# Kernel optimization log

Hardware: AMD Instinct MI355X
Metric: run time of the kernel (lower is better)

Reference implementation:

```python
import jax, jax.numpy as jnp
import numpy as np

NEG = 10000.0

def setup_inputs() -> dict:
    key = jax.random.key(0)
    ks = jax.random.split(key, 5)
    B, S, D = 2, 2048, 1024
    std = 1.0 / np.sqrt(D)
    return {
        "x": jax.random.normal(ks[0], (B, S, D), dtype=jnp.float32),
        "Wq": jax.random.normal(ks[1], (D, D), dtype=jnp.float32) * std,
        "bq": jnp.zeros((D,), jnp.float32),
        "Wk": jax.random.normal(ks[2], (D, D), dtype=jnp.float32) * std,
        "bk": jnp.zeros((D,), jnp.float32),
        "Wv": jax.random.normal(ks[3], (D, D), dtype=jnp.float32) * std,
        "bv": jnp.zeros((D,), jnp.float32),
        "Wo": jax.random.normal(ks[4], (D, D), dtype=jnp.float32) * std,
        "bo": jnp.zeros((D,), jnp.float32),
    }

def reference(x, Wq, bq, Wk, bk, Wv, bv, Wo, bo):
    # Linear projections + relu activation (as in the keras layer; note: no head split
    # is performed in this implementation, head_num is only a divisibility check).
    q = jax.nn.relu(x @ Wq + bq)  # [B,S,D]
    k = jax.nn.relu(x @ Wk + bk)
    v = jax.nn.relu(x @ Wv + bv)
    D = q.shape[-1]
    e = jnp.einsum('bqd,bkd->bqk', q, k) / jnp.sqrt(jnp.float32(D))  # [B,S,S]
    # history_only causal mask: penalize key positions j > query position i
    S = e.shape[-1]
    causal = (jnp.arange(S)[None, :] > jnp.arange(S)[:, None]).astype(e.dtype)
    e = e - NEG * causal[None, :, :]
    # stable softmax exactly as in the source (max-subtract, exp, normalize)
    e = jnp.exp(e - jnp.max(e, axis=-1, keepdims=True))
    attn = e / jnp.sum(e, axis=-1, keepdims=True)
    y = jnp.einsum('bqk,bkd->bqd', attn, v)
    return jax.nn.relu(y @ Wo + bo)
```

## Files before the change

kernel.cpp:

```cpp
#include <hip/hip_runtime.h>
#include <math.h>


typedef _Float16 f16x8 __attribute__((ext_vector_type(8)));
typedef float f32x4 __attribute__((ext_vector_type(4)));

#define BK 64

__device__ __forceinline__ void gload_lds16(const void* g, void* l) {
  __builtin_amdgcn_global_load_lds(
      (const __attribute__((address_space(1))) void*)g,
      (__attribute__((address_space(3))) void*)l, 16, 0, 0);
}

template<bool RELU, bool HAS_BIAS, int CAUSAL, int TMp, int TNp, bool MULTI, typename OT>
__global__ __launch_bounds__(256) void gemm_f16(
    const _Float16* __restrict__ A, const _Float16* __restrict__ BT,
    const float* __restrict__ bias0, const float* __restrict__ bias1,
    const float* __restrict__ bias2,
    OT* __restrict__ C0, OT* __restrict__ C1, OT* __restrict__ C2,
    int M, int Nout, int K, float scale,
    long long sA, long long sB, long long sC)
{
  int m0, n0;
  if (CAUSAL == 1) {
    int bx = blockIdx.x;
    int i = (int)((sqrtf(4.f * bx + 1.f) - 1.f) * 0.5f);
    while ((i + 1) * (i + 2) <= bx) ++i;
    while (i * (i + 1) > bx) --i;
    int j = bx - i * (i + 1);
    m0 = i * TMp;
    n0 = j * TNp;
  } else {
    m0 = blockIdx.y * TMp;
    n0 = blockIdx.x * TNp;
  }
  A  += (long long)blockIdx.z * sA;
  BT += (long long)blockIdx.z * sB;
  const int kend = (CAUSAL == 2) ? ((m0 + TMp < K) ? m0 + TMp : K) : K;

  __shared__ _Float16 Ah[TMp * BK];
  __shared__ _Float16 Bh[TNp * BK];

  const int tid  = threadIdx.x;
  const int lane = tid & 63;
  const int wid  = tid >> 6;
  const int wm   = (wid >> 1) * (TMp / 2);
  const int wn   = (wid & 1) * (TNp / 2);
  const int l15  = lane & 15;
  const int quad = lane >> 4;
  constexpr int MT = TMp / 32;
  constexpr int NT = TNp / 32;

  f32x4 acc[MT][NT];
  #pragma unroll
  for (int i = 0; i < MT; ++i)
    #pragma unroll
    for (int j = 0; j < NT; ++j)
      acc[i][j] = (f32x4){0.f, 0.f, 0.f, 0.f};

  constexpr int AI = TMp / 32;
  constexpr int BI = TNp / 32;
  const int rl8  = lane >> 3;
  const int swk  = ((lane & 7) ^ rl8) * 8;
  const int arow = wid * (TMp / 4);
  const int brow = wid * (TNp / 4);

  for (int k0 = 0; k0 < kend; k0 += BK) {
    #pragma unroll
    for (int t = 0; t < AI; ++t)
      gload_lds16(A + (long long)(m0 + arow + t * 8 + rl8) * K + k0 + swk,
                  Ah + (arow + t * 8) * BK);
    #pragma unroll
    for (int t = 0; t < BI; ++t)
      gload_lds16(BT + (long long)(n0 + brow + t * 8 + rl8) * K + k0 + swk,
                  Bh + (brow + t * 8) * BK);
    __syncthreads();

    const _Float16* ab = Ah + (wm + l15) * BK;
    const _Float16* bb = Bh + (wn + l15) * BK;
    const int sw8 = l15 & 7;
    #pragma unroll
    for (int ko = 0; ko < 2; ++ko) {
      const int ch = ((ko * 4 + quad) ^ sw8) * 8;
      f16x8 af[MT], bf[NT];
      #pragma unroll
      for (int t = 0; t < MT; ++t) af[t] = *(const f16x8*)(ab + t * 16 * BK + ch);
      #pragma unroll
      for (int t = 0; t < NT; ++t) bf[t] = *(const f16x8*)(bb + t * 16 * BK + ch);
      #pragma unroll
      for (int mt = 0; mt < MT; ++mt)
        #pragma unroll
        for (int nt = 0; nt < NT; ++nt)
          acc[mt][nt] = __builtin_amdgcn_mfma_f32_16x16x32_f16(
              af[mt], bf[nt], acc[mt][nt], 0, 0, 0);
    }
    __syncthreads();
  }

  const int mat = MULTI ? (n0 / Nout) : 0;
  const float* bias = HAS_BIAS ? (mat == 0 ? bias0 : (mat == 1 ? bias1 : bias2)) : nullptr;
  OT* C = (mat == 0 ? C0 : (mat == 1 ? C1 : C2)) + (long long)blockIdx.z * sC;
  const int c0 = MULTI ? (n0 - mat * Nout) : n0;

  float bvals[NT];
  if (HAS_BIAS) {
    #pragma unroll
    for (int nt = 0; nt < NT; ++nt)
      bvals[nt] = bias[c0 + wn + nt * 16 + l15];
  }
  #pragma unroll
  for (int mt = 0; mt < MT; ++mt) {
    #pragma unroll
    for (int nt = 0; nt < NT; ++nt) {
      const int col = c0 + wn + nt * 16 + l15;
      #pragma unroll
      for (int r = 0; r < 4; ++r) {
        const int row = m0 + wm + mt * 16 + quad * 4 + r;
        float v = acc[mt][nt][r] * scale;
        if (HAS_BIAS) v += bvals[nt];
        if (RELU) v = fmaxf(v, 0.f);
        C[(long long)row * Nout + col] = (OT)v;
      }
    }
  }
}

__global__ __launch_bounds__(256) void cvt_f32_f16(
    const float* __restrict__ in, _Float16* __restrict__ out)
{
  const long long i = ((long long)blockIdx.x * 256 + threadIdx.x) * 8;
  float4 a = *(const float4*)(in + i);
  float4 b = *(const float4*)(in + i + 4);
  f16x8 o = {(_Float16)a.x, (_Float16)a.y, (_Float16)a.z, (_Float16)a.w,
             (_Float16)b.x, (_Float16)b.y, (_Float16)b.z, (_Float16)b.w};
  *(f16x8*)(out + i) = o;
}

__global__ __launch_bounds__(256) void cvtT_all(
    const float* __restrict__ W0, const float* __restrict__ W1,
    const float* __restrict__ W2, const float* __restrict__ W3,
    _Float16* __restrict__ WT, int K, int N)
{
  __shared__ _Float16 t[64][72];
  const int z = blockIdx.z;
  const float* W = (z == 0) ? W0 : (z == 1) ? W1 : (z == 2) ? W2 : W3;
  _Float16* dst = WT + (long long)z * K * N;
  const int k0 = blockIdx.x * 64, n0 = blockIdx.y * 64;
  const int tid = threadIdx.x;
  #pragma unroll
  for (int it = 0; it < 4; ++it) {
    int idx = tid + it * 256;
    int r = idx >> 4, c4 = (idx & 15) << 2;
    float4 w = *(const float4*)(W + (long long)(k0 + r) * N + n0 + c4);
    t[r][c4 + 0] = (_Float16)w.x; t[r][c4 + 1] = (_Float16)w.y;
    t[r][c4 + 2] = (_Float16)w.z; t[r][c4 + 3] = (_Float16)w.w;
  }
  __syncthreads();
  #pragma unroll
  for (int it = 0; it < 2; ++it) {
    int idx = tid + it * 256;
    int r = idx >> 3, c8 = (idx & 7) << 3;
    f16x8 o;
    #pragma unroll
    for (int j = 0; j < 8; ++j) o[j] = t[c8 + j][r];
    *(f16x8*)(dst + (long long)(n0 + r) * K + k0 + c8) = o;
  }
}

__global__ __launch_bounds__(256) void softmax_causal_h(
    _Float16* __restrict__ E, int S)
{
  const int i = blockIdx.x;
  _Float16* row = E + ((long long)blockIdx.y * S + i) * S;
  const int tid = threadIdx.x;
  const int n = i + 1;
  const int j0 = tid * 8;

  f16x8 hv = *(const f16x8*)(row + j0);
  float vals[8];
  float m = -3.0e38f;
  #pragma unroll
  for (int t = 0; t < 8; ++t) {
    float v = (j0 + t < n) ? (float)hv[t] : -3.0e38f;
    vals[t] = v;
    m = fmaxf(m, v);
  }
  #pragma unroll
  for (int o = 32; o > 0; o >>= 1) m = fmaxf(m, __shfl_down(m, o, 64));

  __shared__ float rmax[4];
  __shared__ float rsum[4];
  const int wave = tid >> 6;
  if ((tid & 63) == 0) rmax[wave] = m;
  __syncthreads();
  m = fmaxf(fmaxf(rmax[0], rmax[1]), fmaxf(rmax[2], rmax[3]));

  float s = 0.f;
  #pragma unroll
  for (int t = 0; t < 8; ++t) {
    float e = (j0 + t < n) ? expf(vals[t] - m) : 0.f;
    vals[t] = e;
    s += e;
  }
  #pragma unroll
  for (int o = 32; o > 0; o >>= 1) s += __shfl_down(s, o, 64);
  if ((tid & 63) == 0) rsum[wave] = s;
  __syncthreads();
  s = rsum[0] + rsum[1] + rsum[2] + rsum[3];

  const float inv = 1.0f / s;
  f16x8 ov;
  #pragma unroll
  for (int t = 0; t < 8; ++t) ov[t] = (_Float16)(vals[t] * inv);
  *(f16x8*)(row + j0) = ov;
}

extern "C" void kernel_launch(void* const* d_in, const int* in_sizes, int n_in,
                              void* d_out, int out_size, void* d_ws, size_t ws_size,
                              hipStream_t stream) {
  const float* x  = (const float*)d_in[0];
  const float* Wq = (const float*)d_in[1];
  const float* bq = (const float*)d_in[2];
  const float* Wk = (const float*)d_in[3];
  const float* bk = (const float*)d_in[4];
  const float* Wv = (const float*)d_in[5];
  const float* bv = (const float*)d_in[6];
  const float* Wo = (const float*)d_in[7];
  const float* bo = (const float*)d_in[8];
  float* out = (float*)d_out;

  const int Bn = 2, S = 2048, D = 1024;
  const int M = Bn * S;
  const size_t MD = (size_t)M * D;
  const size_t DD = (size_t)D * D;
  const size_t SS = (size_t)Bn * S * S;

  _Float16* ws   = (_Float16*)d_ws;
  _Float16* xh   = ws;
  _Float16* Wcat = xh + MD;
  _Float16* Qh   = Wcat + 4 * DD;
  _Float16* Kh   = Qh + MD;
  _Float16* Vh   = Kh + MD;
  _Float16* VWT  = Vh + MD;
  _Float16* E    = VWT + MD;

  dim3 blk(256);

  cvt_f32_f16<<<dim3((unsigned)(MD / 2048)), blk, 0, stream>>>(x, xh);
  cvtT_all<<<dim3(D / 64, D / 64, 4), blk, 0, stream>>>(Wq, Wk, Wv, Wo, Wcat, D, D);

  gemm_f16<true, true, 0, 128, 128, true, _Float16>
      <<<dim3(3 * D / 128, M / 128), blk, 0, stream>>>(
      xh, Wcat, bq, bk, bv, Qh, Kh, Vh, M, D, D, 1.0f, 0, 0, 0);

  gemm_f16<false, false, 1, 128, 64, false, _Float16>
      <<<dim3(272, 1, Bn), blk, 0, stream>>>(
      Qh, Kh, nullptr, nullptr, nullptr, E, nullptr, nullptr,
      S, S, D, 0.03125f, (long long)S * D, (long long)S * D, (long long)S * S);

  gemm_f16<false, false, 0, 128, 64, false, _Float16>
      <<<dim3(S / 64, D / 128, Bn), blk, 0, stream>>>(
      Wcat + 3 * DD, Vh, nullptr, nullptr, nullptr, VWT, nullptr, nullptr,
      D, S, D, 1.0f, 0, (long long)S * D, (long long)D * S);

  softmax_causal_h<<<dim3(S, Bn), blk, 0, stream>>>(E, S);

  gemm_f16<true, true, 2, 64, 128, false, float>
      <<<dim3(D / 128, S / 64, Bn), blk, 0, stream>>>(
      E, VWT, bo, nullptr, nullptr, out, nullptr, nullptr,
      S, D, S, 1.0f, (long long)S * S, (long long)D * S, (long long)S * D);
}
```

Baseline: 209.3 us.

## Merge launches into fused multi-role kernels and halve GEMM K-tile to 32

```diff
diff --git a/kernel.cpp b/kernel.cpp
--- a/kernel.cpp
+++ b/kernel.cpp
@@ -5,7 +5,7 @@
 typedef _Float16 f16x8 __attribute__((ext_vector_type(8)));
 typedef float f32x4 __attribute__((ext_vector_type(4)));
 
-#define BK 64
+#define BK 32
 
 __device__ __forceinline__ void gload_lds16(const void* g, void* l) {
   __builtin_amdgcn_global_load_lds(
@@ -13,35 +13,12 @@
       (__attribute__((address_space(3))) void*)l, 16, 0, 0);
 }
 
-template<bool RELU, bool HAS_BIAS, int CAUSAL, int TMp, int TNp, bool MULTI, typename OT>
-__global__ __launch_bounds__(256) void gemm_f16(
+template<int TMp, int TNp>
+__device__ __forceinline__ void gemm_acc(
     const _Float16* __restrict__ A, const _Float16* __restrict__ BT,
-    const float* __restrict__ bias0, const float* __restrict__ bias1,
-    const float* __restrict__ bias2,
-    OT* __restrict__ C0, OT* __restrict__ C1, OT* __restrict__ C2,
-    int M, int Nout, int K, float scale,
-    long long sA, long long sB, long long sC)
-{
-  int m0, n0;
-  if (CAUSAL == 1) {
-    int bx = blockIdx.x;
-    int i = (int)((sqrtf(4.f * bx + 1.f) - 1.f) * 0.5f);
-    while ((i + 1) * (i + 2) <= bx) ++i;
-    while (i * (i + 1) > bx) --i;
-    int j = bx - i * (i + 1);
-    m0 = i * TMp;
-    n0 = j * TNp;
-  } else {
-    m0 = blockIdx.y * TMp;
-    n0 = blockIdx.x * TNp;
-  }
-  A  += (long long)blockIdx.z * sA;
-  BT += (long long)blockIdx.z * sB;
-  const int kend = (CAUSAL == 2) ? ((m0 + TMp < K) ? m0 + TMp : K) : K;
-
-  __shared__ _Float16 Ah[TMp * BK];
-  __shared__ _Float16 Bh[TNp * BK];
-
+    _Float16* Ah, _Float16* Bh, int sAr, int sBr, int kend, int m0, int n0,
+    f32x4 (&acc)[TMp / 32][TNp / 32])
+{
   const int tid  = threadIdx.x;
   const int lane = tid & 63;
   const int wid  = tid >> 6;
@@ -51,69 +28,68 @@
   const int quad = lane >> 4;
   constexpr int MT = TMp / 32;
   constexpr int NT = TNp / 32;
-
-  f32x4 acc[MT][NT];
-  #pragma unroll
-  for (int i = 0; i < MT; ++i)
-    #pragma unroll
-    for (int j = 0; j < NT; ++j)
-      acc[i][j] = (f32x4){0.f, 0.f, 0.f, 0.f};
-
-  constexpr int AI = TMp / 32;
-  constexpr int BI = TNp / 32;
-  const int rl8  = lane >> 3;
-  const int swk  = ((lane & 7) ^ rl8) * 8;
+  constexpr int AI = TMp / 64;
+  constexpr int BI = TNp / 64;
+  const int r16 = lane >> 2;
+  const int swc = ((lane & 3) ^ ((lane >> 3) & 3)) * 8;
   const int arow = wid * (TMp / 4);
   const int brow = wid * (TNp / 4);
 
   for (int k0 = 0; k0 < kend; k0 += BK) {
     #pragma unroll
     for (int t = 0; t < AI; ++t)
-      gload_lds16(A + (long long)(m0 + arow + t * 8 + rl8) * K + k0 + swk,
-                  Ah + (arow + t * 8) * BK);
+      gload_lds16(A + (long long)(m0 + arow + t * 16 + r16) * sAr + k0 + swc,
+                  Ah + (arow + t * 16) * BK);
     #pragma unroll
     for (int t = 0; t < BI; ++t)
-      gload_lds16(BT + (long long)(n0 + brow + t * 8 + rl8) * K + k0 + swk,
-                  Bh + (brow + t * 8) * BK);
+      gload_lds16(BT + (long long)(n0 + brow + t * 16 + r16) * sBr + k0 + swc,
+                  Bh + (brow + t * 16) * BK);
     __syncthreads();
 
-    const _Float16* ab = Ah + (wm + l15) * BK;
-    const _Float16* bb = Bh + (wn + l15) * BK;
-    const int sw8 = l15 & 7;
-    #pragma unroll
-    for (int ko = 0; ko < 2; ++ko) {
-      const int ch = ((ko * 4 + quad) ^ sw8) * 8;
-      f16x8 af[MT], bf[NT];
+    const int ch = (quad ^ ((l15 >> 1) & 3)) * 8;
+    const _Float16* ab = Ah + (wm + l15) * BK + ch;
+    const _Float16* bb = Bh + (wn + l15) * BK + ch;
+    f16x8 af[MT], bf[NT];
+    #pragma unroll
+    for (int t = 0; t < MT; ++t) af[t] = *(const f16x8*)(ab + t * 16 * BK);
+    #pragma unroll
+    for (int t = 0; t < NT; ++t) bf[t] = *(const f16x8*)(bb + t * 16 * BK);
+    #pragma unroll
+    for (int mt = 0; mt < MT; ++mt)
       #pragma unroll
-      for (int t = 0; t < MT; ++t) af[t] = *(const f16x8*)(ab + t * 16 * BK + ch);
-      #pragma unroll
-      for (int t = 0; t < NT; ++t) bf[t] = *(const f16x8*)(bb + t * 16 * BK + ch);
-      #pragma unroll
-      for (int mt = 0; mt < MT; ++mt)
-        #pragma unroll
-        for (int nt = 0; nt < NT; ++nt)
-          acc[mt][nt] = __builtin_amdgcn_mfma_f32_16x16x32_f16(
-              af[mt], bf[nt], acc[mt][nt], 0, 0, 0);
-    }
+      for (int nt = 0; nt < NT; ++nt)
+        acc[mt][nt] = __builtin_amdgcn_mfma_f32_16x16x32_f16(
+            af[mt], bf[nt], acc[mt][nt], 0, 0, 0);
     __syncthreads();
   }
-
-  const int mat = MULTI ? (n0 / Nout) : 0;
-  const float* bias = HAS_BIAS ? (mat == 0 ? bias0 : (mat == 1 ? bias1 : bias2)) : nullptr;
-  OT* C = (mat == 0 ? C0 : (mat == 1 ? C1 : C2)) + (long long)blockIdx.z * sC;
-  const int c0 = MULTI ? (n0 - mat * Nout) : n0;
+}
+
+template<int TMp, int TNp, bool RELU, bool HAS_BIAS, typename OT>
+__device__ __forceinline__ void gemm_store(
+    f32x4 (&acc)[TMp / 32][TNp / 32], const float* __restrict__ bias,
+    OT* __restrict__ C, int Nout, float scale, int m0, int n0)
+{
+  const int tid  = threadIdx.x;
+  const int lane = tid & 63;
+  const int wid  = tid >> 6;
+  const int wm   = (wid >> 1) * (TMp / 2);
+  const int wn   = (wid & 1) * (TNp / 2);
+  const int l15  = lane & 15;
+  const int quad = lane >> 4;
+  constexpr int MT = TMp / 32;
+  constexpr int NT = TNp / 32;
 
   float bvals[NT];
   if (HAS_BIAS) {
     #pragma unroll
     for (int nt = 0; nt < NT; ++nt)
-      bvals[nt] = bias[c0 + wn + nt * 16 + l15];
+      bvals[nt] = bias[n0 + wn + nt * 16 + l15];
   }
   #pragma unroll
   for (int mt = 0; mt < MT; ++mt) {
     #pragma unroll
     for (int nt = 0; nt < NT; ++nt) {
-      const int col = c0 + wn + nt * 16 + l15;
+      const int col = n0 + wn + nt * 16 + l15;
       #pragma unroll
       for (int r = 0; r < 4; ++r) {
         const int row = m0 + wm + mt * 16 + quad * 4 + r;
@@ -126,33 +102,132 @@
   }
 }
 
-__global__ __launch_bounds__(256) void cvt_f32_f16(
-    const float* __restrict__ in, _Float16* __restrict__ out)
-{
-  const long long i = ((long long)blockIdx.x * 256 + threadIdx.x) * 8;
-  float4 a = *(const float4*)(in + i);
-  float4 b = *(const float4*)(in + i + 4);
-  f16x8 o = {(_Float16)a.x, (_Float16)a.y, (_Float16)a.z, (_Float16)a.w,
-             (_Float16)b.x, (_Float16)b.y, (_Float16)b.z, (_Float16)b.w};
-  *(f16x8*)(out + i) = o;
-}
-
-__global__ __launch_bounds__(256) void cvtT_all(
+__global__ __launch_bounds__(256) void qkv_kernel(
+    const _Float16* __restrict__ xh, const _Float16* __restrict__ Wcat,
+    const float* __restrict__ bq, const float* __restrict__ bk,
+    const float* __restrict__ bv,
+    _Float16* __restrict__ Qh, _Float16* __restrict__ Kh,
+    _Float16* __restrict__ Vh, int D)
+{
+  __shared__ _Float16 Ah[128 * BK];
+  __shared__ _Float16 Bh[128 * BK];
+  const int m0  = blockIdx.y * 128;
+  const int n0g = blockIdx.x * 128;
+  f32x4 acc[4][4];
+  #pragma unroll
+  for (int i = 0; i < 4; ++i)
+    #pragma unroll
+    for (int j = 0; j < 4; ++j) acc[i][j] = (f32x4){0.f, 0.f, 0.f, 0.f};
+
+  gemm_acc<128, 128>(xh, Wcat, Ah, Bh, D, D, D, m0, n0g, acc);
+
+  const int mat = n0g >> 10;
+  const int c0  = n0g & 1023;
+  _Float16* C = (mat == 0) ? Qh : (mat == 1) ? Kh : Vh;
+  const float* bias = (mat == 0) ? bq : (mat == 1) ? bk : bv;
+  gemm_store<128, 128, true, true, _Float16>(acc, bias, C, D, 1.0f, m0, c0);
+}
+
+__global__ __launch_bounds__(256) void mid_kernel(
+    const _Float16* __restrict__ Qh, const _Float16* __restrict__ Kh,
+    _Float16* __restrict__ E, const _Float16* __restrict__ WoT,
+    const _Float16* __restrict__ Vh, _Float16* __restrict__ VWT,
+    int S, int D)
+{
+  __shared__ _Float16 Ah[128 * BK];
+  __shared__ _Float16 Bh[64 * BK];
+  const _Float16 *A, *BT;
+  _Float16* C;
+  int m0, n0;
+  float scale;
+  const int id = blockIdx.x;
+  if (id < 544) {
+    const int z = (id >= 272);
+    const int t = id - z * 272;
+    int i = (int)((sqrtf(4.f * t + 1.f) - 1.f) * 0.5f);
+    while ((i + 1) * (i + 2) <= t) ++i;
+    while (i * (i + 1) > t) --i;
+    const int j = t - i * (i + 1);
+    m0 = i * 128;
+    n0 = j * 64;
+    A  = Qh + (long long)z * S * D;
+    BT = Kh + (long long)z * S * D;
+    C  = E + (long long)z * S * S;
+    scale = 0.03125f;
+  } else {
+    const int t = id - 544;
+    const int z = t >> 8;
+    const int u = t & 255;
+    m0 = (u >> 5) * 128;
+    n0 = (u & 31) * 64;
+    A  = WoT;
+    BT = Vh + (long long)z * S * D;
+    C  = VWT + (long long)z * D * S;
+    scale = 1.0f;
+  }
+  f32x4 acc[4][2];
+  #pragma unroll
+  for (int i = 0; i < 4; ++i)
+    #pragma unroll
+    for (int j = 0; j < 2; ++j) acc[i][j] = (f32x4){0.f, 0.f, 0.f, 0.f};
+
+  gemm_acc<128, 64>(A, BT, Ah, Bh, D, D, D, m0, n0, acc);
+  gemm_store<128, 64, false, false, _Float16>(acc, nullptr, C, S, scale, m0, n0);
+}
+
+__global__ __launch_bounds__(256) void pv_kernel(
+    const _Float16* __restrict__ E, const _Float16* __restrict__ VWT,
+    const float* __restrict__ bo, float* __restrict__ out, int S, int D)
+{
+  __shared__ _Float16 Ah[64 * BK];
+  __shared__ _Float16 Bh[128 * BK];
+  const int z  = blockIdx.z;
+  const int m0 = ((int)gridDim.y - 1 - (int)blockIdx.y) * 64;
+  const int n0 = blockIdx.x * 128;
+  const _Float16* A  = E + (long long)z * S * S;
+  const _Float16* BT = VWT + (long long)z * D * S;
+  float* C = out + (long long)z * S * D;
+  const int kend = m0 + 64;
+
+  f32x4 acc[2][4];
+  #pragma unroll
+  for (int i = 0; i < 2; ++i)
+    #pragma unroll
+    for (int j = 0; j < 4; ++j) acc[i][j] = (f32x4){0.f, 0.f, 0.f, 0.f};
+
+  gemm_acc<64, 128>(A, BT, Ah, Bh, S, S, kend, m0, n0, acc);
+  gemm_store<64, 128, true, true, float>(acc, bo, C, D, 1.0f, m0, n0);
+}
+
+__global__ __launch_bounds__(256) void prep_kernel(
+    const float* __restrict__ x, _Float16* __restrict__ xh,
     const float* __restrict__ W0, const float* __restrict__ W1,
     const float* __restrict__ W2, const float* __restrict__ W3,
-    _Float16* __restrict__ WT, int K, int N)
-{
+    _Float16* __restrict__ Wcat, int D)
+{
+  const int id = blockIdx.x;
+  const int tid = threadIdx.x;
+  if (id < 2048) {
+    const long long i = ((long long)id * 256 + tid) * 8;
+    float4 a = *(const float4*)(x + i);
+    float4 b = *(const float4*)(x + i + 4);
+    f16x8 o = {(_Float16)a.x, (_Float16)a.y, (_Float16)a.z, (_Float16)a.w,
+               (_Float16)b.x, (_Float16)b.y, (_Float16)b.z, (_Float16)b.w};
+    *(f16x8*)(xh + i) = o;
+    return;
+  }
   __shared__ _Float16 t[64][72];
-  const int z = blockIdx.z;
+  const int u = id - 2048;
+  const int z = u >> 8;
+  const int v = u & 255;
   const float* W = (z == 0) ? W0 : (z == 1) ? W1 : (z == 2) ? W2 : W3;
-  _Float16* dst = WT + (long long)z * K * N;
-  const int k0 = blockIdx.x * 64, n0 = blockIdx.y * 64;
-  const int tid = threadIdx.x;
+  _Float16* dst = Wcat + (long long)z * D * D;
+  const int k0 = (v >> 4) * 64, n0 = (v & 15) * 64;
   #pragma unroll
   for (int it = 0; it < 4; ++it) {
     int idx = tid + it * 256;
     int r = idx >> 4, c4 = (idx & 15) << 2;
-    float4 w = *(const float4*)(W + (long long)(k0 + r) * N + n0 + c4);
+    float4 w = *(const float4*)(W + (long long)(k0 + r) * D + n0 + c4);
     t[r][c4 + 0] = (_Float16)w.x; t[r][c4 + 1] = (_Float16)w.y;
     t[r][c4 + 2] = (_Float16)w.z; t[r][c4 + 3] = (_Float16)w.w;
   }
@@ -164,7 +239,7 @@
     f16x8 o;
     #pragma unroll
     for (int j = 0; j < 8; ++j) o[j] = t[c8 + j][r];
-    *(f16x8*)(dst + (long long)(n0 + r) * K + k0 + c8) = o;
+    *(f16x8*)(dst + (long long)(n0 + r) * D + k0 + c8) = o;
   }
 }
 
@@ -247,27 +322,16 @@
 
   dim3 blk(256);
 
-  cvt_f32_f16<<<dim3((unsigned)(MD / 2048)), blk, 0, stream>>>(x, xh);
-  cvtT_all<<<dim3(D / 64, D / 64, 4), blk, 0, stream>>>(Wq, Wk, Wv, Wo, Wcat, D, D);
-
-  gemm_f16<true, true, 0, 128, 128, true, _Float16>
-      <<<dim3(3 * D / 128, M / 128), blk, 0, stream>>>(
-      xh, Wcat, bq, bk, bv, Qh, Kh, Vh, M, D, D, 1.0f, 0, 0, 0);
-
-  gemm_f16<false, false, 1, 128, 64, false, _Float16>
-      <<<dim3(272, 1, Bn), blk, 0, stream>>>(
-      Qh, Kh, nullptr, nullptr, nullptr, E, nullptr, nullptr,
-      S, S, D, 0.03125f, (long long)S * D, (long long)S * D, (long long)S * S);
-
-  gemm_f16<false, false, 0, 128, 64, false, _Float16>
-      <<<dim3(S / 64, D / 128, Bn), blk, 0, stream>>>(
-      Wcat + 3 * DD, Vh, nullptr, nullptr, nullptr, VWT, nullptr, nullptr,
-      D, S, D, 1.0f, 0, (long long)S * D, (long long)D * S);
+  prep_kernel<<<dim3(3072), blk, 0, stream>>>(x, xh, Wq, Wk, Wv, Wo, Wcat, D);
+
+  qkv_kernel<<<dim3(3 * D / 128, M / 128), blk, 0, stream>>>(
+      xh, Wcat, bq, bk, bv, Qh, Kh, Vh, D);
+
+  mid_kernel<<<dim3(1056), blk, 0, stream>>>(
+      Qh, Kh, E, Wcat + 3 * DD, Vh, VWT, S, D);
 
   softmax_causal_h<<<dim3(S, Bn), blk, 0, stream>>>(E, S);
 
-  gemm_f16<true, true, 2, 64, 128, false, float>
-      <<<dim3(D / 128, S / 64, Bn), blk, 0, stream>>>(
-      E, VWT, bo, nullptr, nullptr, out, nullptr, nullptr,
-      S, D, S, 1.0f, (long long)S * S, (long long)D * S, (long long)S * D);
-}
+  pv_kernel<<<dim3(D / 128, S / 64, Bn), blk, 0, stream>>>(
+      E, VWT, bo, out, S, D);
+}
```

Measured after the change: 208.8 us. Within noise of the previous version (-0.3%).
